# Performance work log

Measured on AMD Instinct MI355X. Metric: run time of the kernel, lower is better.

Reference implementation:

```python
import jax, jax.numpy as jnp
import numpy as np
import math

N_NODES, N_EDGES, N_BATCH = 100000, 500000, 256
D_V, D_E, D_U, D_ATTN = 128, 128, 128, 128
NEG = -1e9

def _linear_params(key, fan_in, fan_out):
    kw, kb = jax.random.split(key)
    s = 1.0 / math.sqrt(fan_in)
    W = jax.random.uniform(kw, (fan_in, fan_out), jnp.float32, -s, s)
    b = jax.random.uniform(kb, (fan_out,), jnp.float32, -s, s)
    return W, b

def setup_inputs() -> dict:
    key = jax.random.key(0)
    ks = jax.random.split(key, 10)
    nodes = jax.random.normal(ks[0], (N_NODES, D_V), jnp.float32)
    edges = jax.random.normal(ks[1], (N_EDGES, D_E), jnp.float32)
    edge_index = jax.random.randint(ks[2], (2, N_EDGES), 0, N_NODES, jnp.int64 if jax.config.jax_enable_x64 else jnp.int32)
    u = jax.random.normal(ks[3], (N_BATCH, D_U), jnp.float32)
    batch = jnp.sort(jax.random.randint(ks[4], (N_NODES,), 0, N_BATCH))
    Wq, bq = _linear_params(ks[5], D_E + D_U, D_ATTN)
    Wk, bk = _linear_params(ks[6], D_U, D_ATTN)
    Wv, bv = _linear_params(ks[7], D_E + D_U, D_ATTN)
    Wl, bl = _linear_params(ks[8], D_ATTN, D_E)
    return {"nodes": nodes, "edges": edges, "edge_index": edge_index, "u": u,
            "batch": batch, "Wq": Wq, "bq": bq, "Wk": Wk, "bk": bk,
            "Wv": Wv, "bv": bv, "Wl": Wl, "bl": bl}

def reference(nodes, edges, edge_index, u, batch, Wq, bq, Wk, bk, Wv, bv, Wl, bl):
    lrelu = lambda x: jax.nn.leaky_relu(x, 0.01)  # torch LeakyReLU default slope
    s = edge_index[0]                 # sender node per edge (E,)
    eb = batch[s]                     # graph id per edge (E,)
    x_in = jnp.concatenate([edges, u[eb]], axis=1)   # (E, d_e+d_u)
    q = lrelu(x_in @ Wq + bq)         # (E, d_attn)
    k = lrelu(u @ Wk + bk)            # (B, d_attn)
    v = lrelu(x_in @ Wv + bv)         # (E, d_attn)
    scores = (q @ k.T) / jnp.sqrt(jnp.asarray(q.shape[-1], q.dtype))  # (E, B)
    # block-diagonal batch mask: edge e can attend to graph b iff batch[s[e]]==b
    mask = eb[:, None] == jnp.arange(u.shape[0])[None, :]             # (E, B)
    scores = jnp.where(mask, scores, NEG)
    attn = jax.nn.softmax(scores, axis=0)             # softmax over edges per graph
    x = attn.T @ v                                    # (B, d_attn)
    return lrelu(x @ Wl + bl)                         # (B, d_e)
```

## Files before the change

kernel.cpp:

```cpp
#include <hip/hip_runtime.h>

#define NE 500000
#define NB 256
#define D  128
#define NT 7813
#define GS 2048
#define SPLIT 8
#define APAD 8
#define SCHUNK 1954

typedef __attribute__((ext_vector_type(8))) short bf16x8;
typedef __attribute__((ext_vector_type(4))) float f32x4;

__device__ __forceinline__ float lrelu(float x){ return x > 0.0f ? x : 0.01f * x; }

__device__ __forceinline__ unsigned short f2bf(float f){
  unsigned u = __float_as_uint(f);
  unsigned rounding = 0x7fffu + ((u >> 16) & 1u);
  return (unsigned short)((u + rounding) >> 16);
}

__device__ __forceinline__ unsigned encf(float f){
  unsigned u = __float_as_uint(f);
  return (u & 0x80000000u) ? ~u : (u | 0x80000000u);
}
__device__ __forceinline__ float decf(unsigned u){
  return (u & 0x80000000u) ? __uint_as_float(u & 0x7fffffffu) : __uint_as_float(~u);
}

__global__ void k_init(unsigned* gmax, float* gsum, unsigned* hist){
  int t = threadIdx.x;
  if (t < NB){ gmax[t*APAD] = 0u; gsum[t*APAD] = 0.0f; hist[t*APAD] = 0u; }
}

__global__ void k_pre(const float* __restrict__ u,  const float* __restrict__ Wq,
                      const float* __restrict__ bq, const float* __restrict__ Wk,
                      const float* __restrict__ bk, const float* __restrict__ Wv,
                      const float* __restrict__ bv,
                      float* __restrict__ kT, float* __restrict__ qu, float* __restrict__ vu){
  __shared__ float us[D];
  int b = blockIdx.x, c = threadIdx.x;
  us[c] = u[b*D + c];
  __syncthreads();
  float ka = bk[c], qa = bq[c], va = bv[c];
  #pragma unroll 4
  for (int j = 0; j < D; ++j){
    float uv = us[j];
    ka += uv * Wk[j*D + c];
    qa += uv * Wq[(D + j)*D + c];
    va += uv * Wv[(D + j)*D + c];
  }
  kT[b*D + c] = lrelu(ka);
  qu[b*D + c] = qa;
  vu[b*D + c] = va;
}

__global__ void k_prew(const float* __restrict__ Wq, const float* __restrict__ Wv,
                       unsigned short* __restrict__ WqT, unsigned short* __restrict__ WvT){
  int c = blockIdx.x, k = threadIdx.x;
  WqT[c*D + k] = f2bf(Wq[k*D + c]);
  WvT[c*D + k] = f2bf(Wv[k*D + c]);
}

__device__ __forceinline__ void stage_weights(unsigned short* wt, const unsigned short* Wsrc, int tid){
  const uint4* wsrc = (const uint4*)Wsrc;
  for (int i = tid; i < 2048; i += 256){
    int c = i >> 4, off = (i & 15) << 4;
    *(uint4*)((char*)wt + c*256 + (off ^ ((c & 7) << 4))) = wsrc[i];
  }
}

__device__ __forceinline__ void stage_edge_row(unsigned short* xs, const float* __restrict__ edges,
                                               long e, int r, int q){
  const float4* src = (const float4*)(edges + (size_t)e * D + q * 32);
  char* xrow = (char*)xs + r * 256;
  #pragma unroll
  for (int ci = 0; ci < 4; ++ci){
    float4 a = src[2*ci], b = src[2*ci + 1];
    bf16x8 pk;
    pk[0] = (short)f2bf(a.x); pk[1] = (short)f2bf(a.y);
    pk[2] = (short)f2bf(a.z); pk[3] = (short)f2bf(a.w);
    pk[4] = (short)f2bf(b.x); pk[5] = (short)f2bf(b.y);
    pk[6] = (short)f2bf(b.z); pk[7] = (short)f2bf(b.w);
    int off = q * 64 + ci * 16;
    *(bf16x8*)(xrow + (off ^ ((r & 7) << 4))) = pk;
  }
}

__device__ __forceinline__ void mfma_tile(f32x4 acc[8], const unsigned short* xs,
                                          const unsigned short* wt, int w, int g, int m){
  const int arow = 16 * w + m;
  #pragma unroll
  for (int ks = 0; ks < 4; ++ks){
    int koff = ks * 64 + (g << 4);
    bf16x8 af = *(const bf16x8*)((const char*)xs + arow*256 + (koff ^ ((arow & 7) << 4)));
    #pragma unroll
    for (int n = 0; n < 8; ++n){
      int bc = 16 * n + m;
      bf16x8 bv = *(const bf16x8*)((const char*)wt + bc*256 + (koff ^ ((bc & 7) << 4)));
      acc[n] = __builtin_amdgcn_mfma_f32_16x16x32_bf16(af, bv, acc[n], 0, 0, 0);
    }
  }
}

__global__ __launch_bounds__(256)
void k_score(const float* __restrict__ edges, const int* __restrict__ send,
             const int* __restrict__ batch, const unsigned short* __restrict__ WqT,
             const float* __restrict__ qu, const float* __restrict__ kT,
             float* __restrict__ scores, int* __restrict__ ebArr){
  __shared__ __align__(16) unsigned short wt[D * D];
  __shared__ __align__(16) unsigned short xs[64 * D];
  __shared__ int ebs[64];
  const int tid = threadIdx.x;
  stage_weights(wt, WqT, tid);
  const int lane = tid & 63, w = tid >> 6, g = lane >> 4, m = lane & 15;
  const int r = tid >> 2, q = tid & 3;

  for (int t = blockIdx.x; t < NT; t += GS){
    __syncthreads();
    const int base = t * 64;
    if (tid < 64){
      int e  = base + tid;
      int ec = e < NE ? e : NE - 1;
      int eb = batch[send[ec]];
      ebs[tid] = eb;
      if (e < NE) ebArr[e] = eb;
    }
    {
      int e = base + r; if (e >= NE) e = NE - 1;
      stage_edge_row(xs, edges, e, r, q);
    }
    __syncthreads();

    int ebj[4];
    #pragma unroll
    for (int j = 0; j < 4; ++j) ebj[j] = ebs[16*w + 4*g + j];
    f32x4 acc[8];
    #pragma unroll
    for (int n = 0; n < 8; ++n){
      #pragma unroll
      for (int j = 0; j < 4; ++j)
        acc[n][j] = qu[(size_t)ebj[j] * D + 16*n + m];
    }
    mfma_tile(acc, xs, wt, w, g, m);

    #pragma unroll
    for (int j = 0; j < 4; ++j){
      float p = 0.0f;
      const float* krow = kT + (size_t)ebj[j] * D;
      #pragma unroll
      for (int n = 0; n < 8; ++n)
        p += lrelu(acc[n][j]) * krow[16*n + m];
      p += __shfl_xor(p, 1); p += __shfl_xor(p, 2);
      p += __shfl_xor(p, 4); p += __shfl_xor(p, 8);
      int eg = base + 16*w + 4*g + j;
      if (m == 0 && eg < NE) scores[eg] = p * 0.08838834764831843f;
    }
  }
}

__global__ __launch_bounds__(256)
void k_stats(const float* __restrict__ scores, const int* __restrict__ ebArr,
             unsigned* gmax, unsigned* hist){
  __shared__ unsigned lmax[NB];
  __shared__ unsigned lcnt[NB];
  int tid = threadIdx.x;
  lmax[tid] = 0u; lcnt[tid] = 0u;
  __syncthreads();
  int start = blockIdx.x * SCHUNK;
  int end = start + SCHUNK; if (end > NE) end = NE;
  for (int e = start + tid; e < end; e += 256){
    int b = ebArr[e];
    atomicMax(&lmax[b], encf(scores[e]));
    atomicAdd(&lcnt[b], 1u);
  }
  __syncthreads();
  unsigned c = lcnt[tid];
  if (c){ atomicAdd(&hist[tid*APAD], c); atomicMax(&gmax[tid*APAD], lmax[tid]); }
}

__global__ void k_scan(const unsigned* __restrict__ hist, unsigned* __restrict__ offs,
                       unsigned* cursor){
  __shared__ unsigned sh[NB];
  __shared__ unsigned so[NB + 1];
  int tid = threadIdx.x;
  sh[tid] = hist[tid*APAD];
  __syncthreads();
  if (tid == 0){
    unsigned run = 0;
    for (int b = 0; b < NB; ++b){ so[b] = run; run += sh[b]; }
    so[NB] = run;
  }
  __syncthreads();
  offs[tid] = so[tid];
  cursor[tid*APAD] = so[tid];
  if (tid == 0) offs[NB] = so[NB];
}

__global__ __launch_bounds__(256)
void k_scatter(const float* __restrict__ scores, const int* __restrict__ ebArr,
               const unsigned* __restrict__ gmax, unsigned* cursor,
               unsigned* __restrict__ perm, float* gsum){
  __shared__ unsigned lbase[NB];
  __shared__ unsigned lcnt[NB];
  __shared__ float lsum[NB];
  __shared__ float lgm[NB];
  int tid = threadIdx.x;
  lcnt[tid] = 0u; lsum[tid] = 0.0f; lgm[tid] = decf(gmax[tid*APAD]);
  __syncthreads();
  int start = blockIdx.x * SCHUNK;
  int end = start + SCHUNK; if (end > NE) end = NE;
  for (int e = start + tid; e < end; e += 256)
    atomicAdd(&lcnt[ebArr[e]], 1u);
  __syncthreads();
  unsigned c = lcnt[tid];
  lbase[tid] = c ? atomicAdd(&cursor[tid*APAD], c) : 0u;
  lcnt[tid] = 0u;
  __syncthreads();
  for (int e = start + tid; e < end; e += 256){
    int b = ebArr[e];
    unsigned p = lbase[b] + atomicAdd(&lcnt[b], 1u);
    perm[p] = (unsigned)e;
    atomicAdd(&lsum[b], __expf(scores[e] - lgm[b]));
  }
  __syncthreads();
  if (lsum[tid] != 0.0f) atomicAdd(&gsum[tid*APAD], lsum[tid]);
}

__global__ __launch_bounds__(256)
void k_accum(const float* __restrict__ edges, const unsigned short* __restrict__ WvT,
             const float* __restrict__ vu, const float* __restrict__ scores,
             const unsigned* __restrict__ gmax, const unsigned* __restrict__ offs,
             const unsigned* __restrict__ perm, float* __restrict__ xpart){
  __shared__ __align__(16) unsigned short wt[D * D];
  __shared__ __align__(16) unsigned short xs[64 * D];
  __shared__ float wlds[64];
  __shared__ unsigned el[64];
  __shared__ float xred[4 * D];
  const int tid = threadIdx.x;
  const int b = blockIdx.x >> 3, chunk = blockIdx.x & (SPLIT - 1);
  const unsigned o0 = offs[b];
  const int count = (int)(offs[b + 1] - o0);
  stage_weights(wt, WvT, tid);
  const float gm = decf(gmax[b*APAD]);
  const int lane = tid & 63, w = tid >> 6, g = lane >> 4, m = lane & 15;
  const int r = tid >> 2, q = tid & 3;
  float vureg[8];
  #pragma unroll
  for (int n = 0; n < 8; ++n) vureg[n] = vu[(size_t)b * D + 16*n + m];
  float xacc[8] = {0,0,0,0,0,0,0,0};

  const int ntile = (count + 63) >> 6;
  for (int t = chunk; t < ntile; t += SPLIT){
    __syncthreads();
    if (tid < 64){
      int slot = t * 64 + tid;
      int sc_ = slot < count ? slot : count - 1;
      unsigned e = perm[o0 + sc_];
      el[tid] = e;
      wlds[tid] = slot < count ? __expf(scores[e] - gm) : 0.0f;
    }
    __syncthreads();
    stage_edge_row(xs, edges, (long)el[r], r, q);
    __syncthreads();

    f32x4 acc[8];
    #pragma unroll
    for (int n = 0; n < 8; ++n){
      acc[n][0] = vureg[n]; acc[n][1] = vureg[n];
      acc[n][2] = vureg[n]; acc[n][3] = vureg[n];
    }
    mfma_tile(acc, xs, wt, w, g, m);

    #pragma unroll
    for (int j = 0; j < 4; ++j){
      float wlj = wlds[16*w + 4*g + j];
      #pragma unroll
      for (int n = 0; n < 8; ++n)
        xacc[n] += wlj * lrelu(acc[n][j]);
    }
  }
  #pragma unroll
  for (int n = 0; n < 8; ++n){
    float v = xacc[n];
    v += __shfl_xor(v, 16);
    v += __shfl_xor(v, 32);
    if (g == 0) xred[w * D + 16*n + m] = v;
  }
  __syncthreads();
  if (tid < D){
    float s = xred[tid] + xred[D + tid] + xred[2*D + tid] + xred[3*D + tid];
    xpart[((size_t)b * SPLIT + chunk) * D + tid] = s;
  }
}

__global__ void k_final(const float* __restrict__ xpart, const float* __restrict__ gsum,
                        const float* __restrict__ Wl, const float* __restrict__ bl,
                        float* __restrict__ out){
  __shared__ float xr[D];
  int b = blockIdx.x, c = threadIdx.x;
  float gs = gsum[b*APAD];
  float s = 0.0f;
  #pragma unroll
  for (int ch = 0; ch < SPLIT; ++ch) s += xpart[((size_t)b * SPLIT + ch) * D + c];
  xr[c] = gs > 0.0f ? s / gs : 0.0f;
  __syncthreads();
  float a = bl[c];
  #pragma unroll 4
  for (int j = 0; j < D; ++j) a += xr[j] * Wl[j*D + c];
  out[(size_t)b * D + c] = lrelu(a);
}

extern "C" void kernel_launch(void* const* d_in, const int* in_sizes, int n_in,
                              void* d_out, int out_size, void* d_ws, size_t ws_size,
                              hipStream_t stream){
  const float* edges = (const float*)d_in[1];
  const int*   send  = (const int*)d_in[2];
  const float* u     = (const float*)d_in[3];
  const int*   batch = (const int*)d_in[4];
  const float* Wq    = (const float*)d_in[5];
  const float* bq    = (const float*)d_in[6];
  const float* Wk    = (const float*)d_in[7];
  const float* bk    = (const float*)d_in[8];
  const float* Wv    = (const float*)d_in[9];
  const float* bv    = (const float*)d_in[10];
  const float* Wl    = (const float*)d_in[11];
  const float* bl    = (const float*)d_in[12];
  float* out = (float*)d_out;

  char* wsb = (char*)d_ws;
  size_t off = 0;
  auto alloc = [&](size_t bytes)->char*{
    char* p = wsb + off; off += (bytes + 255) & ~(size_t)255; return p;
  };
  float*    kT     = (float*)   alloc((size_t)NB * D * 4);
  float*    qu     = (float*)   alloc((size_t)NB * D * 4);
  float*    vu     = (float*)   alloc((size_t)NB * D * 4);
  unsigned* gmax   = (unsigned*)alloc((size_t)NB * APAD * 4);
  float*    gsum   = (float*)   alloc((size_t)NB * APAD * 4);
  unsigned* hist   = (unsigned*)alloc((size_t)NB * APAD * 4);
  unsigned* cursor = (unsigned*)alloc((size_t)NB * APAD * 4);
  unsigned* offs   = (unsigned*)alloc((size_t)(NB + 1) * 4);
  unsigned short* WqTb = (unsigned short*)alloc((size_t)D * D * 2);
  unsigned short* WvTb = (unsigned short*)alloc((size_t)D * D * 2);
  float*    xpart  = (float*)   alloc((size_t)NB * SPLIT * D * 4);
  float*    scores = (float*)   alloc((size_t)NE * 4);
  int*      ebArr  = (int*)     alloc((size_t)NE * 4);
  unsigned* perm   = (unsigned*)alloc((size_t)NE * 4);
  (void)ws_size; (void)in_sizes; (void)n_in; (void)out_size;

  k_init   <<<1, 256, 0, stream>>>(gmax, gsum, hist);
  k_pre    <<<NB, D, 0, stream>>>(u, Wq, bq, Wk, bk, Wv, bv, kT, qu, vu);
  k_prew   <<<D, D, 0, stream>>>(Wq, Wv, WqTb, WvTb);
  k_score  <<<GS, 256, 0, stream>>>(edges, send, batch, WqTb, qu, kT, scores, ebArr);
  k_stats  <<<256, 256, 0, stream>>>(scores, ebArr, gmax, hist);
  k_scan   <<<1, 256, 0, stream>>>(hist, offs, cursor);
  k_scatter<<<256, 256, 0, stream>>>(scores, ebArr, gmax, cursor, perm, gsum);
  k_accum  <<<NB * SPLIT, 256, 0, stream>>>(edges, WvTb, vu, scores, gmax, offs, perm, xpart);
  k_final  <<<NB, D, 0, stream>>>(xpart, gsum, Wl, bl, out);
}
```

Measured before the change: 202.0 us.

## Fuse Q and V projections into one edge pass and stream bf16 V to accumulation

```diff
diff --git a/kernel.cpp b/kernel.cpp
--- a/kernel.cpp
+++ b/kernel.cpp
@@ -4,8 +4,8 @@
 #define NB 256
 #define D  128
 #define NT 7813
-#define GS 2048
-#define SPLIT 8
+#define GMAIN 1024
+#define SPLIT 16
 #define APAD 8
 #define SCHUNK 1954
 
@@ -70,13 +70,19 @@
   }
 }
 
-__device__ __forceinline__ void stage_edge_row(unsigned short* xs, const float* __restrict__ edges,
-                                               long e, int r, int q){
+__device__ __forceinline__ void load_rows(float4 pf[8], const float* __restrict__ edges,
+                                          int t, int r, int q){
+  long e = (long)t * 64 + r; if (e >= NE) e = NE - 1;
   const float4* src = (const float4*)(edges + (size_t)e * D + q * 32);
+  #pragma unroll
+  for (int i = 0; i < 8; ++i) pf[i] = src[i];
+}
+
+__device__ __forceinline__ void conv_rows(unsigned short* xs, const float4 pf[8], int r, int q){
   char* xrow = (char*)xs + r * 256;
   #pragma unroll
   for (int ci = 0; ci < 4; ++ci){
-    float4 a = src[2*ci], b = src[2*ci + 1];
+    float4 a = pf[2*ci], b = pf[2*ci + 1];
     bf16x8 pk;
     pk[0] = (short)f2bf(a.x); pk[1] = (short)f2bf(a.y);
     pk[2] = (short)f2bf(a.z); pk[3] = (short)f2bf(a.w);
@@ -87,94 +93,100 @@
   }
 }
 
-__device__ __forceinline__ void mfma_tile(f32x4 acc[8], const unsigned short* xs,
-                                          const unsigned short* wt, int w, int g, int m){
-  const int arow = 16 * w + m;
-  #pragma unroll
-  for (int ks = 0; ks < 4; ++ks){
-    int koff = ks * 64 + (g << 4);
-    bf16x8 af = *(const bf16x8*)((const char*)xs + arow*256 + (koff ^ ((arow & 7) << 4)));
-    #pragma unroll
-    for (int n = 0; n < 8; ++n){
-      int bc = 16 * n + m;
-      bf16x8 bv = *(const bf16x8*)((const char*)wt + bc*256 + (koff ^ ((bc & 7) << 4)));
-      acc[n] = __builtin_amdgcn_mfma_f32_16x16x32_bf16(af, bv, acc[n], 0, 0, 0);
-    }
-  }
-}
-
 __global__ __launch_bounds__(256)
-void k_score(const float* __restrict__ edges, const int* __restrict__ send,
-             const int* __restrict__ batch, const unsigned short* __restrict__ WqT,
-             const float* __restrict__ qu, const float* __restrict__ kT,
-             float* __restrict__ scores, int* __restrict__ ebArr){
-  __shared__ __align__(16) unsigned short wt[D * D];
-  __shared__ __align__(16) unsigned short xs[64 * D];
-  __shared__ int ebs[64];
+void k_main(const float* __restrict__ edges, const int* __restrict__ send,
+            const int* __restrict__ batch, const unsigned short* __restrict__ WqT,
+            const unsigned short* __restrict__ WvT, const float* __restrict__ qu,
+            const float* __restrict__ vu, const float* __restrict__ kT,
+            float* __restrict__ scores, int* __restrict__ ebArr,
+            unsigned short* __restrict__ vprime, unsigned* gmax, unsigned* hist){
+  __shared__ __align__(16) unsigned short wq[D * D];
+  __shared__ __align__(16) unsigned short wv[D * D];
+  __shared__ __align__(16) unsigned short xs[2][64 * D];
+  __shared__ int ebs[2][64];
+  __shared__ unsigned lmax[NB], lcnt[NB];
+
   const int tid = threadIdx.x;
-  stage_weights(wt, WqT, tid);
+  stage_weights(wq, WqT, tid);
+  stage_weights(wv, WvT, tid);
+  lmax[tid] = 0u; lcnt[tid] = 0u;
+
   const int lane = tid & 63, w = tid >> 6, g = lane >> 4, m = lane & 15;
   const int r = tid >> 2, q = tid & 3;
 
-  for (int t = blockIdx.x; t < NT; t += GS){
-    __syncthreads();
-    const int base = t * 64;
+  float4 pf[8];
+  int svp = 0;
+  const int t0 = blockIdx.x;
+  load_rows(pf, edges, t0, r, q);
+  if (tid < 64){ long e = (long)t0 * 64 + tid; if (e >= NE) e = NE - 1; svp = send[e]; }
+  int cur = 0;
+
+  for (int t = t0; t < NT; t += GMAIN, cur ^= 1){
+    conv_rows(xs[cur], pf, r, q);
     if (tid < 64){
-      int e  = base + tid;
-      int ec = e < NE ? e : NE - 1;
-      int eb = batch[send[ec]];
-      ebs[tid] = eb;
+      int eb = batch[svp];
+      ebs[cur][tid] = eb;
+      long e = (long)t * 64 + tid;
       if (e < NE) ebArr[e] = eb;
     }
-    {
-      int e = base + r; if (e >= NE) e = NE - 1;
-      stage_edge_row(xs, edges, e, r, q);
+    int tn = t + GMAIN;
+    if (tn < NT){
+      load_rows(pf, edges, tn, r, q);
+      if (tid < 64){ long e = (long)tn * 64 + tid; if (e >= NE) e = NE - 1; svp = send[e]; }
     }
     __syncthreads();
 
     int ebj[4];
     #pragma unroll
-    for (int j = 0; j < 4; ++j) ebj[j] = ebs[16*w + 4*g + j];
-    f32x4 acc[8];
+    for (int j = 0; j < 4; ++j) ebj[j] = ebs[cur][16*w + 4*g + j];
+    f32x4 qa[8], va[8];
     #pragma unroll
     for (int n = 0; n < 8; ++n){
       #pragma unroll
-      for (int j = 0; j < 4; ++j)
-        acc[n][j] = qu[(size_t)ebj[j] * D + 16*n + m];
-    }
-    mfma_tile(acc, xs, wt, w, g, m);
-
+      for (int j = 0; j < 4; ++j){
+        qa[n][j] = qu[(size_t)ebj[j] * D + 16*n + m];
+        va[n][j] = vu[(size_t)ebj[j] * D + 16*n + m];
+      }
+    }
+    const int arow = 16*w + m;
+    #pragma unroll
+    for (int ks = 0; ks < 4; ++ks){
+      int koff = ks * 64 + (g << 4);
+      bf16x8 af = *(const bf16x8*)((const char*)xs[cur] + arow*256 + (koff ^ ((arow & 7) << 4)));
+      #pragma unroll
+      for (int n = 0; n < 8; ++n){
+        int bc = 16*n + m;
+        int boff = koff ^ ((bc & 7) << 4);
+        bf16x8 bqf = *(const bf16x8*)((const char*)wq + bc*256 + boff);
+        qa[n] = __builtin_amdgcn_mfma_f32_16x16x32_bf16(af, bqf, qa[n], 0, 0, 0);
+        bf16x8 bvf = *(const bf16x8*)((const char*)wv + bc*256 + boff);
+        va[n] = __builtin_amdgcn_mfma_f32_16x16x32_bf16(af, bvf, va[n], 0, 0, 0);
+      }
+    }
     #pragma unroll
     for (int j = 0; j < 4; ++j){
+      int er = 16*w + 4*g + j;
+      long e = (long)t * 64 + er;
+      bf16x8 pk;
+      #pragma unroll
+      for (int n = 0; n < 8; ++n) pk[n] = (short)f2bf(lrelu(va[n][j]));
+      if (e < NE) *(bf16x8*)(vprime + (size_t)e * D + m*8) = pk;
+
       float p = 0.0f;
       const float* krow = kT + (size_t)ebj[j] * D;
       #pragma unroll
-      for (int n = 0; n < 8; ++n)
-        p += lrelu(acc[n][j]) * krow[16*n + m];
+      for (int n = 0; n < 8; ++n) p += lrelu(qa[n][j]) * krow[16*n + m];
       p += __shfl_xor(p, 1); p += __shfl_xor(p, 2);
       p += __shfl_xor(p, 4); p += __shfl_xor(p, 8);
-      int eg = base + 16*w + 4*g + j;
-      if (m == 0 && eg < NE) scores[eg] = p * 0.08838834764831843f;
-    }
-  }
-}
-
-__global__ __launch_bounds__(256)
-void k_stats(const float* __restrict__ scores, const int* __restrict__ ebArr,
-             unsigned* gmax, unsigned* hist){
-  __shared__ unsigned lmax[NB];
-  __shared__ unsigned lcnt[NB];
-  int tid = threadIdx.x;
-  lmax[tid] = 0u; lcnt[tid] = 0u;
-  __syncthreads();
-  int start = blockIdx.x * SCHUNK;
-  int end = start + SCHUNK; if (end > NE) end = NE;
-  for (int e = start + tid; e < end; e += 256){
-    int b = ebArr[e];
-    atomicMax(&lmax[b], encf(scores[e]));
-    atomicAdd(&lcnt[b], 1u);
-  }
-  __syncthreads();
+      if (m == 0 && e < NE){
+        float sc = p * 0.08838834764831843f;
+        scores[e] = sc;
+        atomicMax(&lmax[ebj[j]], encf(sc));
+        atomicAdd(&lcnt[ebj[j]], 1u);
+      }
+    }
+    __syncthreads();
+  }
   unsigned c = lcnt[tid];
   if (c){ atomicAdd(&hist[tid*APAD], c); atomicMax(&gmax[tid*APAD], lmax[tid]); }
 }
@@ -228,65 +240,29 @@
 }
 
 __global__ __launch_bounds__(256)
-void k_accum(const float* __restrict__ edges, const unsigned short* __restrict__ WvT,
-             const float* __restrict__ vu, const float* __restrict__ scores,
-             const unsigned* __restrict__ gmax, const unsigned* __restrict__ offs,
-             const unsigned* __restrict__ perm, float* __restrict__ xpart){
-  __shared__ __align__(16) unsigned short wt[D * D];
-  __shared__ __align__(16) unsigned short xs[64 * D];
-  __shared__ float wlds[64];
-  __shared__ unsigned el[64];
+void k_accum2(const unsigned* __restrict__ vp32, const float* __restrict__ scores,
+              const unsigned* __restrict__ gmax, const unsigned* __restrict__ offs,
+              const unsigned* __restrict__ perm, float* __restrict__ xpart){
   __shared__ float xred[4 * D];
   const int tid = threadIdx.x;
-  const int b = blockIdx.x >> 3, chunk = blockIdx.x & (SPLIT - 1);
+  const int b = blockIdx.x >> 4, chunk = blockIdx.x & (SPLIT - 1);
   const unsigned o0 = offs[b];
   const int count = (int)(offs[b + 1] - o0);
-  stage_weights(wt, WvT, tid);
+  const int r0 = (int)(((long)count * chunk) / SPLIT);
+  const int r1 = (int)(((long)count * (chunk + 1)) / SPLIT);
   const float gm = decf(gmax[b*APAD]);
-  const int lane = tid & 63, w = tid >> 6, g = lane >> 4, m = lane & 15;
-  const int r = tid >> 2, q = tid & 3;
-  float vureg[8];
-  #pragma unroll
-  for (int n = 0; n < 8; ++n) vureg[n] = vu[(size_t)b * D + 16*n + m];
-  float xacc[8] = {0,0,0,0,0,0,0,0};
-
-  const int ntile = (count + 63) >> 6;
-  for (int t = chunk; t < ntile; t += SPLIT){
-    __syncthreads();
-    if (tid < 64){
-      int slot = t * 64 + tid;
-      int sc_ = slot < count ? slot : count - 1;
-      unsigned e = perm[o0 + sc_];
-      el[tid] = e;
-      wlds[tid] = slot < count ? __expf(scores[e] - gm) : 0.0f;
-    }
-    __syncthreads();
-    stage_edge_row(xs, edges, (long)el[r], r, q);
-    __syncthreads();
-
-    f32x4 acc[8];
-    #pragma unroll
-    for (int n = 0; n < 8; ++n){
-      acc[n][0] = vureg[n]; acc[n][1] = vureg[n];
-      acc[n][2] = vureg[n]; acc[n][3] = vureg[n];
-    }
-    mfma_tile(acc, xs, wt, w, g, m);
-
-    #pragma unroll
-    for (int j = 0; j < 4; ++j){
-      float wlj = wlds[16*w + 4*g + j];
-      #pragma unroll
-      for (int n = 0; n < 8; ++n)
-        xacc[n] += wlj * lrelu(acc[n][j]);
-    }
-  }
-  #pragma unroll
-  for (int n = 0; n < 8; ++n){
-    float v = xacc[n];
-    v += __shfl_xor(v, 16);
-    v += __shfl_xor(v, 32);
-    if (g == 0) xred[w * D + 16*n + m] = v;
-  }
+  const int lane = tid & 63, w = tid >> 6;
+  float xa = 0.0f, xb = 0.0f;
+  #pragma unroll 4
+  for (int i = r0 + w; i < r1; i += 4){
+    unsigned e = perm[o0 + i];
+    float we = __expf(scores[e] - gm);
+    unsigned d = vp32[(size_t)e * 64 + lane];
+    xa += we * __uint_as_float(d << 16);
+    xb += we * __uint_as_float(d & 0xffff0000u);
+  }
+  xred[w * D + 2*lane]     = xa;
+  xred[w * D + 2*lane + 1] = xb;
   __syncthreads();
   if (tid < D){
     float s = xred[tid] + xred[D + tid] + xred[2*D + tid] + xred[3*D + tid];
@@ -307,7 +283,10 @@
   __syncthreads();
   float a = bl[c];
   #pragma unroll 4
-  for (int j = 0; j < D; ++j) a += xr[j] * Wl[j*D + c];
+  for (int j = 0; j < D; ++j){
+    float xv = xr[((j & 15) << 3) + (j >> 4)];
+    a += xv * Wl[j*D + c];
+  }
   out[(size_t)b * D + c] = lrelu(a);
 }
 
@@ -347,15 +326,16 @@
   float*    scores = (float*)   alloc((size_t)NE * 4);
   int*      ebArr  = (int*)     alloc((size_t)NE * 4);
   unsigned* perm   = (unsigned*)alloc((size_t)NE * 4);
+  unsigned short* vprime = (unsigned short*)alloc((size_t)NE * D * 2);
   (void)ws_size; (void)in_sizes; (void)n_in; (void)out_size;
 
   k_init   <<<1, 256, 0, stream>>>(gmax, gsum, hist);
   k_pre    <<<NB, D, 0, stream>>>(u, Wq, bq, Wk, bk, Wv, bv, kT, qu, vu);
   k_prew   <<<D, D, 0, stream>>>(Wq, Wv, WqTb, WvTb);
-  k_score  <<<GS, 256, 0, stream>>>(edges, send, batch, WqTb, qu, kT, scores, ebArr);
-  k_stats  <<<256, 256, 0, stream>>>(scores, ebArr, gmax, hist);
+  k_main   <<<GMAIN, 256, 0, stream>>>(edges, send, batch, WqTb, WvTb, qu, vu, kT,
+                                       scores, ebArr, vprime, gmax, hist);
   k_scan   <<<1, 256, 0, stream>>>(hist, offs, cursor);
   k_scatter<<<256, 256, 0, stream>>>(scores, ebArr, gmax, cursor, perm, gsum);
-  k_accum  <<<NB * SPLIT, 256, 0, stream>>>(edges, WvTb, vu, scores, gmax, offs, perm, xpart);
+  k_accum2 <<<NB * SPLIT, 256, 0, stream>>>((const unsigned*)vprime, scores, gmax, offs, perm, xpart);
   k_final  <<<NB, D, 0, stream>>>(xpart, gsum, Wl, bl, out);
 }
```

New measurement: 275.6 us. 1.36x slower.
